# Kernel tuning notes

Measured on AMD Instinct MI355X. Metric: run time of the kernel, lower is better.

The kernel has to match this reference:

```python
import jax, jax.numpy as jnp
import numpy as np

N = 50000      # nodes
E = 800000     # edges
G = 2000       # graphs
F_IN = 34
HID = 256
H = 8
D = 32         # HID // H
L = 5


def _layer_norm(x, g, b, eps=1e-5):
    m = x.mean(-1, keepdims=True)
    v = ((x - m) ** 2).mean(-1, keepdims=True)
    return (x - m) / jnp.sqrt(v + eps) * g + b


def _gelu(x):
    return jax.nn.gelu(x, approximate=False)  # torch exact GELU


def _segment_softmax(scores, seg, n):
    # scores: [E', H], seg: [E'] target node ids
    m = jax.ops.segment_max(scores, seg, num_segments=n)
    m = jnp.where(jnp.isfinite(m), m, 0.0)
    ex = jnp.exp(scores - m[seg])
    den = jax.ops.segment_sum(ex, seg, num_segments=n)
    return ex / (den[seg] + 1e-16)


def setup_inputs() -> dict:
    key = jax.random.key(0)
    ks = iter(jax.random.split(key, 64))

    def p(shape, fan):
        return (jax.random.normal(next(ks), shape, jnp.float32) / np.sqrt(fan)).astype(jnp.float32)

    inp = {}
    inp['x'] = jax.random.normal(next(ks), (N, F_IN), jnp.float32)
    inp['edge_index'] = jax.random.randint(next(ks), (2, E), 0, N, jnp.int32)
    inp['batch'] = jnp.sort(jax.random.randint(next(ks), (N,), 0, G, jnp.int32))

    # input embed
    inp['in_W'] = p((F_IN, HID), F_IN); inp['in_b'] = jnp.zeros((HID,), jnp.float32)
    inp['in_ln_g'] = jnp.ones((HID,), jnp.float32); inp['in_ln_b'] = jnp.zeros((HID,), jnp.float32)
    # 5 GATv2 layers (stacked on leading dim)
    inp['gat_Wl'] = p((L, HID, HID), HID); inp['gat_bl'] = jnp.zeros((L, HID), jnp.float32)
    inp['gat_Wr'] = p((L, HID, HID), HID); inp['gat_br'] = jnp.zeros((L, HID), jnp.float32)
    inp['gat_att'] = p((L, H, D), D)
    inp['gat_bias'] = jnp.zeros((L, HID), jnp.float32)
    inp['gat_ln_g'] = jnp.ones((L, HID), jnp.float32); inp['gat_ln_b'] = jnp.zeros((L, HID), jnp.float32)
    # TransformerConv
    inp['tr_Wq'] = p((HID, HID), HID); inp['tr_bq'] = jnp.zeros((HID,), jnp.float32)
    inp['tr_Wk'] = p((HID, HID), HID); inp['tr_bk'] = jnp.zeros((HID,), jnp.float32)
    inp['tr_Wv'] = p((HID, HID), HID); inp['tr_bv'] = jnp.zeros((HID,), jnp.float32)
    inp['tr_Wskip'] = p((HID, HID), HID); inp['tr_bskip'] = jnp.zeros((HID,), jnp.float32)
    inp['tr_ln_g'] = jnp.ones((HID,), jnp.float32); inp['tr_ln_b'] = jnp.zeros((HID,), jnp.float32)
    # output proj
    inp['out_W'] = p((2 * HID, 2 * HID), 2 * HID); inp['out_b'] = jnp.zeros((2 * HID,), jnp.float32)
    inp['out_ln_g'] = jnp.ones((2 * HID,), jnp.float32); inp['out_ln_b'] = jnp.zeros((2 * HID,), jnp.float32)
    return inp


def reference(x, edge_index, batch,
              in_W, in_b, in_ln_g, in_ln_b,
              gat_Wl, gat_bl, gat_Wr, gat_br, gat_att, gat_bias, gat_ln_g, gat_ln_b,
              tr_Wq, tr_bq, tr_Wk, tr_bk, tr_Wv, tr_bv, tr_Wskip, tr_bskip, tr_ln_g, tr_ln_b,
              out_W, out_b, out_ln_g, out_ln_b):
    # input embedding (dropout inactive in eval)
    h = _gelu(_layer_norm(x @ in_W + in_b, in_ln_g, in_ln_b))

    src, dst = edge_index[0], edge_index[1]  # PyG: row=source j, col=target i
    loops = jnp.arange(N, dtype=src.dtype)
    s2 = jnp.concatenate([src, loops])  # GATv2 adds self loops
    d2 = jnp.concatenate([dst, loops])

    for l in range(L):  # small fixed loop over layers
        xl = (h @ gat_Wl[l] + gat_bl[l]).reshape(N, H, D)  # source transform / message
        xr = (h @ gat_Wr[l] + gat_br[l]).reshape(N, H, D)  # target transform
        e = jax.nn.leaky_relu(xl[s2] + xr[d2], 0.2)        # [E', H, D]
        score = jnp.einsum('ehd,hd->eh', e, gat_att[l])
        alpha = _segment_softmax(score, d2, N)             # softmax over incoming edges
        out = jax.ops.segment_sum(xl[s2] * alpha[..., None], d2, num_segments=N)
        out = out.reshape(N, HID) + gat_bias[l]
        h = h + _gelu(_layer_norm(out, gat_ln_g[l], gat_ln_b[l]))

    # TransformerConv (no self loops, root_weight skip connection)
    q = (h @ tr_Wq + tr_bq).reshape(N, H, D)
    k = (h @ tr_Wk + tr_bk).reshape(N, H, D)
    v = (h @ tr_Wv + tr_bv).reshape(N, H, D)
    score = (q[dst] * k[src]).sum(-1) / jnp.sqrt(jnp.float32(D))  # [E, H]
    alpha = _segment_softmax(score, dst, N)
    out = jax.ops.segment_sum(v[src] * alpha[..., None], dst, num_segments=N).reshape(N, HID)
    out = out + h @ tr_Wskip + tr_bskip
    h = h + _layer_norm(out, tr_ln_g, tr_ln_b)

    # global mean + max pool
    cnt = jax.ops.segment_sum(jnp.ones((N,), h.dtype), batch, num_segments=G)
    h_mean = jax.ops.segment_sum(h, batch, num_segments=G) / jnp.maximum(cnt, 1.0)[:, None]
    h_max = jax.ops.segment_max(h, batch, num_segments=G)
    h_max = jnp.where(jnp.isfinite(h_max), h_max, 0.0)
    ge = jnp.concatenate([h_mean, h_max], axis=-1)  # [G, 512]
    return _gelu(_layer_norm(ge @ out_W + out_b, out_ln_g, out_ln_b))
```

## Files before the change

kernel.cpp:

```cpp
#include <hip/hip_runtime.h>
#include <math.h>

#define N_NODES 50000
#define N_EDGES 800000
#define N_GRAPH 2000
#define F_INPUT 34
#define HID 256
#define NLAYER 5

typedef __attribute__((ext_vector_type(8))) short short8;
typedef __attribute__((ext_vector_type(4))) float float4v;

__device__ __forceinline__ float gelu_f(float x) {
  return 0.5f * x * (1.0f + erff(x * 0.70710678118654752440f));
}
__device__ __forceinline__ unsigned short bfr(float f) {
  unsigned u = __float_as_uint(f);
  return (unsigned short)((u + 0x7fffu + ((u >> 16) & 1u)) >> 16);
}
__device__ __forceinline__ float b2f(unsigned short s) {
  return __uint_as_float(((unsigned)s) << 16);
}
__device__ __forceinline__ float4 ld4bf(const unsigned short* p) {
  ushort4 u = *(const ushort4*)p;
  float4 f;
  f.x = b2f(u.x); f.y = b2f(u.y); f.z = b2f(u.z); f.w = b2f(u.w);
  return f;
}
__device__ __forceinline__ void acp16(const unsigned short* g, unsigned short* l) {
  __builtin_amdgcn_global_load_lds(
      (const __attribute__((address_space(1))) void*)g,
      (__attribute__((address_space(3))) void*)l, 16, 0, 0);
}

__global__ __launch_bounds__(256) void gemm_bias(
    const float* __restrict__ A, const float* __restrict__ B,
    const float* __restrict__ bias, float* __restrict__ C,
    int M, int Nn, int K) {
  __shared__ float As[16][64];
  __shared__ float Bs[16][64];
  int tid = threadIdx.x;
  int tx = tid & 15, ty = tid >> 4;
  int row0 = blockIdx.y * 64;
  int col0 = blockIdx.x * 64;
  float acc[4][4] = {};
  int a_r = tid >> 2;
  int a_c = (tid & 3) * 4;
  int b_r = tid >> 4;
  int b_c = (tid & 15) * 4;

  for (int k0 = 0; k0 < K; k0 += 16) {
    int ar = row0 + a_r;
#pragma unroll
    for (int i = 0; i < 4; ++i) {
      int kc = k0 + a_c + i;
      As[a_c + i][a_r] = (ar < M && kc < K) ? A[(long)ar * K + kc] : 0.f;
    }
    int bk = k0 + b_r;
    if (bk < K) {
      float4 bv = *(const float4*)&B[(long)bk * Nn + col0 + b_c];
      Bs[b_r][b_c + 0] = bv.x; Bs[b_r][b_c + 1] = bv.y;
      Bs[b_r][b_c + 2] = bv.z; Bs[b_r][b_c + 3] = bv.w;
    } else {
      Bs[b_r][b_c + 0] = 0.f; Bs[b_r][b_c + 1] = 0.f;
      Bs[b_r][b_c + 2] = 0.f; Bs[b_r][b_c + 3] = 0.f;
    }
    __syncthreads();
#pragma unroll
    for (int kk = 0; kk < 16; ++kk) {
      float4 a = *(const float4*)&As[kk][ty * 4];
      float4 b = *(const float4*)&Bs[kk][tx * 4];
      float av[4] = {a.x, a.y, a.z, a.w};
      float bv[4] = {b.x, b.y, b.z, b.w};
#pragma unroll
      for (int i = 0; i < 4; ++i)
#pragma unroll
        for (int j = 0; j < 4; ++j) acc[i][j] += av[i] * bv[j];
    }
    __syncthreads();
  }
  float4 bi = *(const float4*)&bias[col0 + tx * 4];
  float bia[4] = {bi.x, bi.y, bi.z, bi.w};
#pragma unroll
  for (int i = 0; i < 4; ++i) {
    int r = row0 + ty * 4 + i;
    if (r < M) {
      float4 o;
      o.x = acc[i][0] + bia[0]; o.y = acc[i][1] + bia[1];
      o.z = acc[i][2] + bia[2]; o.w = acc[i][3] + bia[3];
      *(float4*)&C[(long)r * Nn + col0 + tx * 4] = o;
    }
  }
}

__global__ __launch_bounds__(256) void gemm_mfma(
    const unsigned short* __restrict__ A, const unsigned short* __restrict__ Bt,
    const float* __restrict__ bias, void* __restrict__ Cv,
    int M, int Nn, int K, int flags) {
  __shared__ unsigned short smem[12288];
  unsigned short* As = smem;
  unsigned short* Bs = smem + 4096;
  int tid = threadIdx.x;
  int wave = tid >> 6, lane = tid & 63;
  int row0 = blockIdx.y * 128;
  int col0 = blockIdx.x * 128;
  int wm0 = (wave >> 1) * 64;
  int wn0 = (wave & 1) * 64;
  int q = lane >> 4;
  int ln = lane & 15;

  int srow = wave * 16 + (lane >> 2);
  int scol = (lane & 3) * 8;
  int ra0 = min(row0 + srow, M - 1);
  int ra1 = min(row0 + srow + 64, M - 1);
  const unsigned short* pa0 = A + (size_t)ra0 * K + scol;
  const unsigned short* pa1 = A + (size_t)ra1 * K + scol;
  const unsigned short* pb0 = Bt + (size_t)(col0 + srow) * K + scol;
  const unsigned short* pb1 = Bt + (size_t)(col0 + srow + 64) * K + scol;
  unsigned short* la0 = As + wave * 512;
  unsigned short* la1 = As + wave * 512 + 2048;
  unsigned short* lb0 = Bs + wave * 512;
  unsigned short* lb1 = Bs + wave * 512 + 2048;

  float4v acc[4][4];
#pragma unroll
  for (int i = 0; i < 4; ++i)
#pragma unroll
    for (int j = 0; j < 4; ++j) acc[i][j] = (float4v)0.f;

  for (int k0 = 0; k0 < K; k0 += 32) {
    acp16(pa0 + k0, la0);
    acp16(pa1 + k0, la1);
    acp16(pb0 + k0, lb0);
    acp16(pb1 + k0, lb1);
    __syncthreads();
    short8 af[4], bf[4];
#pragma unroll
    for (int i = 0; i < 4; ++i)
      af[i] = *(const short8*)&As[(wm0 + i * 16 + ln) * 32 + q * 8];
#pragma unroll
    for (int j = 0; j < 4; ++j)
      bf[j] = *(const short8*)&Bs[(wn0 + j * 16 + ln) * 32 + q * 8];
#pragma unroll
    for (int i = 0; i < 4; ++i)
#pragma unroll
      for (int j = 0; j < 4; ++j)
        acc[i][j] = __builtin_amdgcn_mfma_f32_16x16x32_bf16(af[i], bf[j], acc[i][j], 0, 0, 0);
    __syncthreads();
  }
  int rb = (lane >> 4) * 4;
  if (flags & 2) {
    unsigned short* Cb = (unsigned short*)Cv;
    unsigned short* eb = smem + wave * 2560;
#pragma unroll
    for (int p = 0; p < 2; ++p) {
#pragma unroll
      for (int jj = 0; jj < 2; ++jj) {
        int j = p * 2 + jj;
        float bv = bias[col0 + wn0 + j * 16 + ln];
#pragma unroll
        for (int i = 0; i < 4; ++i)
#pragma unroll
          for (int r = 0; r < 4; ++r)
            eb[(i * 16 + rb + r) * 40 + jj * 16 + ln] = bfr(acc[i][j][r] + bv);
      }
      int grow = row0 + wm0 + lane;
      uint4 w0 = *(uint4*)&eb[lane * 40 + 0];
      uint4 w1 = *(uint4*)&eb[lane * 40 + 8];
      uint4 w2 = *(uint4*)&eb[lane * 40 + 16];
      uint4 w3 = *(uint4*)&eb[lane * 40 + 24];
      if (grow < M) {
        unsigned short* dst = Cb + (size_t)grow * Nn + col0 + wn0 + p * 32;
        *(uint4*)&dst[0] = w0;
        *(uint4*)&dst[8] = w1;
        *(uint4*)&dst[16] = w2;
        *(uint4*)&dst[24] = w3;
      }
    }
  } else {
    float* C = (float*)Cv;
#pragma unroll
    for (int j = 0; j < 4; ++j) {
      int col = col0 + wn0 + j * 16 + ln;
      float bv = bias[col];
#pragma unroll
      for (int i = 0; i < 4; ++i)
#pragma unroll
        for (int r = 0; r < 4; ++r) {
          int row = row0 + wm0 + i * 16 + rb + r;
          if (row < M) C[(size_t)row * Nn + col] = acc[i][j][r] + bv;
        }
    }
  }
}

__global__ __launch_bounds__(256) void prep_w(
    const float* __restrict__ Wl, const float* __restrict__ Wr,
    const float* __restrict__ Wq, const float* __restrict__ Wk,
    const float* __restrict__ Wv, const float* __restrict__ Wsk,
    unsigned short* __restrict__ out) {
  __shared__ float t[32][33];
  int m = blockIdx.z;
  const float* W = (m < 10) ? (((m & 1) ? Wr : Wl) + (size_t)(m >> 1) * 65536)
                 : (m == 10) ? Wq : (m == 11) ? Wk : (m == 12) ? Wv : Wsk;
  int k0 = blockIdx.y * 32, n0 = blockIdx.x * 32;
  int r = threadIdx.x >> 5, c = threadIdx.x & 31;
  for (int rr = r; rr < 32; rr += 8)
    t[rr][c] = W[(size_t)(k0 + rr) * HID + n0 + c];
  __syncthreads();
  unsigned short* o = out + (size_t)m * 65536;
  for (int rr = r; rr < 32; rr += 8)
    o[(size_t)(n0 + rr) * HID + k0 + c] = bfr(t[c][rr]);
}

__global__ __launch_bounds__(256) void prep_wout(const float* __restrict__ W,
                                                 unsigned short* __restrict__ o) {
  __shared__ float t[32][33];
  int k0 = blockIdx.y * 32, n0 = blockIdx.x * 32;
  int r = threadIdx.x >> 5, c = threadIdx.x & 31;
  for (int rr = r; rr < 32; rr += 8)
    t[rr][c] = W[(size_t)(k0 + rr) * 512 + n0 + c];
  __syncthreads();
  for (int rr = r; rr < 32; rr += 8)
    o[(size_t)(n0 + rr) * 512 + k0 + c] = bfr(t[c][rr]);
}

__global__ __launch_bounds__(256) void prep_bias(
    const float* __restrict__ bl, const float* __restrict__ br,
    const float* __restrict__ bq, const float* __restrict__ bk,
    const float* __restrict__ bv, float* __restrict__ out) {
  int i = blockIdx.x * 256 + threadIdx.x;
  if (i < 2560) {
    int l = i >> 9, c = i & 511;
    out[i] = (c < 256) ? bl[l * 256 + c] : br[l * 256 + (c - 256)];
  } else if (i < 3328) {
    int j = i - 2560;
    out[i] = (j < 256) ? bq[j] : (j < 512) ? bk[j - 256] : bv[j - 512];
  }
}

__global__ __launch_bounds__(256) void ln_act(
    const float* __restrict__ in, const float* __restrict__ gam,
    const float* __restrict__ bet, float* __restrict__ out,
    unsigned short* __restrict__ outb,
    int n_rows, int width, int do_gelu) {
  int wid = blockIdx.x * 4 + (threadIdx.x >> 6);
  int lane = threadIdx.x & 63;
  if (wid >= n_rows) return;
  int chunks = width >> 8;
  float4 v[2];
  float s = 0.f;
  for (int c = 0; c < chunks; ++c) {
    int off = c * 256 + lane * 4;
    float4 t = *(const float4*)&in[(size_t)wid * width + off];
    v[c] = t;
    s += t.x + t.y + t.z + t.w;
  }
  for (int o = 1; o < 64; o <<= 1) s += __shfl_xor(s, o);
  float mean = s / (float)width;
  float vs = 0.f;
  for (int c = 0; c < chunks; ++c) {
    float dx = v[c].x - mean, dy = v[c].y - mean, dz = v[c].z - mean, dw = v[c].w - mean;
    vs += dx * dx + dy * dy + dz * dz + dw * dw;
  }
  for (int o = 1; o < 64; o <<= 1) vs += __shfl_xor(vs, o);
  float inv = rsqrtf(vs / (float)width + 1e-5f);
  for (int c = 0; c < chunks; ++c) {
    int off = c * 256 + lane * 4;
    float4 g4 = *(const float4*)&gam[off];
    float4 b4 = *(const float4*)&bet[off];
    float y[4] = {(v[c].x - mean) * inv * g4.x + b4.x,
                  (v[c].y - mean) * inv * g4.y + b4.y,
                  (v[c].z - mean) * inv * g4.z + b4.z,
                  (v[c].w - mean) * inv * g4.w + b4.w};
    if (do_gelu) {
#pragma unroll
      for (int i = 0; i < 4; ++i) y[i] = gelu_f(y[i]);
    }
    size_t idx = (size_t)wid * width + off;
    float4 o4 = {y[0], y[1], y[2], y[3]};
    *(float4*)&out[idx] = o4;
    if (outb) {
      ushort4 ob = {bfr(y[0]), bfr(y[1]), bfr(y[2]), bfr(y[3])};
      *(ushort4*)&outb[idx] = ob;
    }
  }
}

__global__ __launch_bounds__(256) void edge_count(const int* __restrict__ ei,
                                                  int* __restrict__ counts) {
  int e = blockIdx.x * 256 + threadIdx.x;
  if (e < N_EDGES) atomicAdd(&counts[ei[N_EDGES + e]], 1);
}

__global__ __launch_bounds__(1024) void scan1(const int* __restrict__ counts,
                                              int* __restrict__ indptr,
                                              int* __restrict__ bsums, int n) {
  __shared__ int sm[1024];
  int tid = threadIdx.x;
  int i = blockIdx.x * 1024 + tid;
  int v = (i < n) ? counts[i] : 0;
  sm[tid] = v;
  __syncthreads();
  for (int off = 1; off < 1024; off <<= 1) {
    int t = (tid >= off) ? sm[tid - off] : 0;
    __syncthreads();
    sm[tid] += t;
    __syncthreads();
  }
  if (i < n) indptr[i] = sm[tid] - v;
  if (tid == 1023) bsums[blockIdx.x] = sm[1023];
}

__global__ void scan2(int* __restrict__ bsums, int nb) {
  if (threadIdx.x == 0 && blockIdx.x == 0) {
    int acc = 0;
    for (int i = 0; i < nb; ++i) { int t = bsums[i]; bsums[i] = acc; acc += t; }
  }
}

__global__ __launch_bounds__(256) void scan3(const int* __restrict__ bsums,
                                             int* __restrict__ indptr,
                                             int* __restrict__ cursor, int n) {
  int i = blockIdx.x * 256 + threadIdx.x;
  if (i < n) {
    int v = indptr[i] + bsums[i >> 10];
    indptr[i] = v;
    cursor[i] = v;
  }
  if (i == 0) indptr[n] = N_EDGES;
}

__global__ __launch_bounds__(256) void edge_scatter(const int* __restrict__ ei,
                                                    int* __restrict__ cursor,
                                                    int* __restrict__ esrc) {
  int e = blockIdx.x * 256 + threadIdx.x;
  if (e < N_EDGES) {
    int d = ei[N_EDGES + e];
    int p = atomicAdd(&cursor[d], 1);
    esrc[p] = ei[e];
  }
}

#define GAT_EDGE(f)                                                        \
  {                                                                        \
    float ex = f.x + xri.x; ex = ex > 0.f ? ex : 0.2f * ex;                \
    float ey = f.y + xri.y; ey = ey > 0.f ? ey : 0.2f * ey;                \
    float ez = f.z + xri.z; ez = ez > 0.f ? ez : 0.2f * ez;                \
    float ew = f.w + xri.w; ew = ew > 0.f ? ew : 0.2f * ew;                \
    float p = ex * a4.x + ey * a4.y + ez * a4.z + ew * a4.w;               \
    p += __shfl_xor(p, 1); p += __shfl_xor(p, 2); p += __shfl_xor(p, 4);   \
    float wgt = __expf(fminf(p - m0, 60.f));                               \
    ax += wgt * f.x; ay += wgt * f.y; az += wgt * f.z; aw += wgt * f.w;    \
    lsum += wgt;                                                           \
  }

__global__ __launch_bounds__(256) void gat_agg(
    const unsigned short* __restrict__ xlr, const float* __restrict__ att,
    const int* __restrict__ indptr, const int* __restrict__ esrc,
    const float* __restrict__ pre_bias, const float* __restrict__ gam,
    const float* __restrict__ bet, float* __restrict__ h,
    unsigned short* __restrict__ hb) {
  int wid = blockIdx.x * 4 + (threadIdx.x >> 6);
  int lane = threadIdx.x & 63;
  if (wid >= N_NODES) return;
  float4 xri = ld4bf(&xlr[(size_t)wid * 512 + 256 + lane * 4]);
  float4 a4 = *(const float4*)&att[lane * 4];
  int beg = indptr[wid], end = indptr[wid + 1];

  float m0, lsum, ax, ay, az, aw;
  {
    float4 f = ld4bf(&xlr[(size_t)wid * 512 + lane * 4]);
    float ex = f.x + xri.x; ex = ex > 0.f ? ex : 0.2f * ex;
    float ey = f.y + xri.y; ey = ey > 0.f ? ey : 0.2f * ey;
    float ez = f.z + xri.z; ez = ez > 0.f ? ez : 0.2f * ez;
    float ew = f.w + xri.w; ew = ew > 0.f ? ew : 0.2f * ew;
    float p = ex * a4.x + ey * a4.y + ez * a4.z + ew * a4.w;
    p += __shfl_xor(p, 1); p += __shfl_xor(p, 2); p += __shfl_xor(p, 4);
    m0 = p; lsum = 1.f;
    ax = f.x; ay = f.y; az = f.z; aw = f.w;
  }
  int e = beg;
  for (; e + 3 < end; e += 4) {
    int j0 = esrc[e], j1 = esrc[e + 1], j2 = esrc[e + 2], j3 = esrc[e + 3];
    float4 f0 = ld4bf(&xlr[(size_t)j0 * 512 + lane * 4]);
    float4 f1 = ld4bf(&xlr[(size_t)j1 * 512 + lane * 4]);
    float4 f2 = ld4bf(&xlr[(size_t)j2 * 512 + lane * 4]);
    float4 f3 = ld4bf(&xlr[(size_t)j3 * 512 + lane * 4]);
    GAT_EDGE(f0); GAT_EDGE(f1); GAT_EDGE(f2); GAT_EDGE(f3);
  }
  for (; e < end; ++e) {
    int j = esrc[e];
    float4 f = ld4bf(&xlr[(size_t)j * 512 + lane * 4]);
    GAT_EDGE(f);
  }
  float inv = 1.f / (lsum + 1e-16f);
  float4 pb = *(const float4*)&pre_bias[lane * 4];
  float y0 = ax * inv + pb.x, y1 = ay * inv + pb.y;
  float y2 = az * inv + pb.z, y3 = aw * inv + pb.w;
  float s = y0 + y1 + y2 + y3;
  for (int o = 1; o < 64; o <<= 1) s += __shfl_xor(s, o);
  float mean = s * (1.f / 256.f);
  float d0 = y0 - mean, d1 = y1 - mean, d2 = y2 - mean, d3 = y3 - mean;
  float vs = d0 * d0 + d1 * d1 + d2 * d2 + d3 * d3;
  for (int o = 1; o < 64; o <<= 1) vs += __shfl_xor(vs, o);
  float inv2 = rsqrtf(vs * (1.f / 256.f) + 1e-5f);
  float4 g4 = *(const float4*)&gam[lane * 4];
  float4 b4 = *(const float4*)&bet[lane * 4];
  y0 = gelu_f(d0 * inv2 * g4.x + b4.x);
  y1 = gelu_f(d1 * inv2 * g4.y + b4.y);
  y2 = gelu_f(d2 * inv2 * g4.z + b4.z);
  y3 = gelu_f(d3 * inv2 * g4.w + b4.w);
  size_t idx = (size_t)wid * HID + lane * 4;
  float4 r4 = *(const float4*)&h[idx];
  y0 += r4.x; y1 += r4.y; y2 += r4.z; y3 += r4.w;
  float4 o4 = {y0, y1, y2, y3};
  *(float4*)&h[idx] = o4;
  ushort4 ob = {bfr(y0), bfr(y1), bfr(y2), bfr(y3)};
  *(ushort4*)&hb[idx] = ob;
}

#define TR_EDGE(kj, vj)                                                    \
  {                                                                        \
    float p = qi.x * kj.x + qi.y * kj.y + qi.z * kj.z + qi.w * kj.w;       \
    p += __shfl_xor(p, 1); p += __shfl_xor(p, 2); p += __shfl_xor(p, 4);   \
    float wgt = __expf(fminf(p * scale, 60.f));                            \
    ax += wgt * vj.x; ay += wgt * vj.y; az += wgt * vj.z; aw += wgt * vj.w;\
    lsum += wgt;                                                           \
  }

__global__ __launch_bounds__(256) void tr_agg(
    const unsigned short* __restrict__ qkv, const int* __restrict__ indptr,
    const int* __restrict__ esrc, const unsigned short* __restrict__ skipb,
    const float* __restrict__ gam, const float* __restrict__ bet,
    float* __restrict__ h) {
  int wid = blockIdx.x * 4 + (threadIdx.x >> 6);
  int lane = threadIdx.x & 63;
  if (wid >= N_NODES) return;
  float4 qi = ld4bf(&qkv[(size_t)wid * 768 + lane * 4]);
  int beg = indptr[wid], end = indptr[wid + 1];
  float lsum = 0.f;
  float ax = 0.f, ay = 0.f, az = 0.f, aw = 0.f;
  const float scale = 0.17677669529663687f;
  int e = beg;
  for (; e + 1 < end; e += 2) {
    int j0 = esrc[e], j1 = esrc[e + 1];
    float4 k0 = ld4bf(&qkv[(size_t)j0 * 768 + 256 + lane * 4]);
    float4 v0 = ld4bf(&qkv[(size_t)j0 * 768 + 512 + lane * 4]);
    float4 k1 = ld4bf(&qkv[(size_t)j1 * 768 + 256 + lane * 4]);
    float4 v1 = ld4bf(&qkv[(size_t)j1 * 768 + 512 + lane * 4]);
    TR_EDGE(k0, v0); TR_EDGE(k1, v1);
  }
  if (e < end) {
    int j = esrc[e];
    float4 kj = ld4bf(&qkv[(size_t)j * 768 + 256 + lane * 4]);
    float4 vj = ld4bf(&qkv[(size_t)j * 768 + 512 + lane * 4]);
    TR_EDGE(kj, vj);
  }
  float inv = 1.f / (lsum + 1e-16f);
  size_t idx = (size_t)wid * HID + lane * 4;
  float4 sk = ld4bf(&skipb[idx]);
  float y0 = ax * inv + sk.x, y1 = ay * inv + sk.y;
  float y2 = az * inv + sk.z, y3 = aw * inv + sk.w;
  float s = y0 + y1 + y2 + y3;
  for (int o = 1; o < 64; o <<= 1) s += __shfl_xor(s, o);
  float mean = s * (1.f / 256.f);
  float d0 = y0 - mean, d1 = y1 - mean, d2 = y2 - mean, d3 = y3 - mean;
  float vs = d0 * d0 + d1 * d1 + d2 * d2 + d3 * d3;
  for (int o = 1; o < 64; o <<= 1) vs += __shfl_xor(vs, o);
  float inv2 = rsqrtf(vs * (1.f / 256.f) + 1e-5f);
  float4 g4 = *(const float4*)&gam[lane * 4];
  float4 b4 = *(const float4*)&bet[lane * 4];
  float4 r4 = *(const float4*)&h[idx];
  float4 o4;
  o4.x = r4.x + d0 * inv2 * g4.x + b4.x;
  o4.y = r4.y + d1 * inv2 * g4.y + b4.y;
  o4.z = r4.z + d2 * inv2 * g4.z + b4.z;
  o4.w = r4.w + d3 * inv2 * g4.w + b4.w;
  *(float4*)&h[idx] = o4;
}

__global__ __launch_bounds__(256) void graph_bounds(const int* __restrict__ batch,
                                                    int* __restrict__ gptr) {
  int i = blockIdx.x * 256 + threadIdx.x;
  if (i >= N_NODES) return;
  int b0 = batch[i];
  if (i == 0)
    for (int g = 0; g <= b0; ++g) gptr[g] = 0;
  int b1 = (i + 1 < N_NODES) ? batch[i + 1] : N_GRAPH;
  for (int g = b0 + 1; g <= b1; ++g) gptr[g] = i + 1;
}

__global__ __launch_bounds__(256) void pool_seg(
    const float* __restrict__ h, const int* __restrict__ gptr,
    unsigned short* __restrict__ geb) {
  int g = blockIdx.x, c = threadIdx.x;
  int s = gptr[g], e = gptr[g + 1];
  float sum = 0.f, mx = -INFINITY;
  for (int r = s; r < e; ++r) {
    float vv = h[(size_t)r * HID + c];
    sum += vv;
    mx = fmaxf(mx, vv);
  }
  int cnt = e - s;
  geb[(size_t)g * 512 + c] = bfr(sum / (float)max(cnt, 1));
  geb[(size_t)g * 512 + 256 + c] = bfr(cnt ? mx : 0.f);
}

static inline void mfma_launch(const unsigned short* A, const unsigned short* Bt,
                               const float* bias, void* C, int M, int Nn, int K,
                               int flags, hipStream_t s) {
  dim3 grid(Nn / 128, (M + 127) / 128);
  gemm_mfma<<<grid, 256, 0, s>>>(A, Bt, bias, C, M, Nn, K, flags);
}

extern "C" void kernel_launch(void* const* d_in, const int* in_sizes, int n_in,
                              void* d_out, int out_size, void* d_ws, size_t ws_size,
                              hipStream_t stream) {
  const float* x       = (const float*)d_in[0];
  const int*   ei      = (const int*)d_in[1];
  const int*   batch   = (const int*)d_in[2];
  const float* in_W    = (const float*)d_in[3];
  const float* in_b    = (const float*)d_in[4];
  const float* in_ln_g = (const float*)d_in[5];
  const float* in_ln_b = (const float*)d_in[6];
  const float* gat_Wl  = (const float*)d_in[7];
  const float* gat_bl  = (const float*)d_in[8];
  const float* gat_Wr  = (const float*)d_in[9];
  const float* gat_br  = (const float*)d_in[10];
  const float* gat_att = (const float*)d_in[11];
  const float* gat_bias= (const float*)d_in[12];
  const float* gat_ln_g= (const float*)d_in[13];
  const float* gat_ln_b= (const float*)d_in[14];
  const float* tr_Wq   = (const float*)d_in[15];
  const float* tr_bq   = (const float*)d_in[16];
  const float* tr_Wk   = (const float*)d_in[17];
  const float* tr_bk   = (const float*)d_in[18];
  const float* tr_Wv   = (const float*)d_in[19];
  const float* tr_bv   = (const float*)d_in[20];
  const float* tr_Wsk  = (const float*)d_in[21];
  const float* tr_bsk  = (const float*)d_in[22];
  const float* tr_ln_g = (const float*)d_in[23];
  const float* tr_ln_b = (const float*)d_in[24];
  const float* out_W   = (const float*)d_in[25];
  const float* out_b   = (const float*)d_in[26];
  const float* out_ln_g= (const float*)d_in[27];
  const float* out_ln_b= (const float*)d_in[28];

  char* w = (char*)d_ws;
  auto take = [&](size_t bytes) -> char* {
    char* p = w;
    w += (bytes + 255) & ~(size_t)255;
    return p;
  };
  const size_t NB = (size_t)N_NODES * HID * sizeof(float);
  float* h    = (float*)take(NB);
  float* aggO = (float*)take(NB);
  unsigned short* hb  = (unsigned short*)take((size_t)N_NODES * HID * 2);
  unsigned short* xq  = (unsigned short*)take((size_t)N_NODES * 768 * 2);
  unsigned short* wbuf= (unsigned short*)take((size_t)(14 * 65536 + 262144) * 2);
  float* bcat = (float*)take(3328 * sizeof(float));
  int* indptr = (int*)take((N_NODES + 1) * sizeof(int));
  int* cursor = (int*)take(N_NODES * sizeof(int));
  int* counts = (int*)take(N_NODES * sizeof(int));
  int* esrc   = (int*)take(N_EDGES * sizeof(int));
  int* bsums  = (int*)take(64 * sizeof(int));
  unsigned short* skipb = (unsigned short*)aggO;
  char* w2 = (char*)xq;
  auto take2 = [&](size_t bytes) -> char* {
    char* p = w2;
    w2 += (bytes + 255) & ~(size_t)255;
    return p;
  };
  int* gptr = (int*)take2((N_GRAPH + 1) * sizeof(int));
  unsigned short* geb = (unsigned short*)take2((size_t)N_GRAPH * 512 * 2);
  float* tbuf = (float*)take2((size_t)N_GRAPH * 512 * sizeof(float));

  const int EB = (N_EDGES + 255) / 256;
  const int WB = (N_NODES + 3) / 4;
  const int NSB = (N_NODES + 1023) / 1024;

  {
    dim3 g(8, 8, 14);
    prep_w<<<g, 256, 0, stream>>>(gat_Wl, gat_Wr, tr_Wq, tr_Wk, tr_Wv, tr_Wsk, wbuf);
    dim3 g2(16, 16);
    prep_wout<<<g2, 256, 0, stream>>>(out_W, wbuf + (size_t)14 * 65536);
    prep_bias<<<13, 256, 0, stream>>>(gat_bl, gat_br, tr_bq, tr_bk, tr_bv, bcat);
  }

  hipMemsetAsync(counts, 0, N_NODES * sizeof(int), stream);
  edge_count<<<EB, 256, 0, stream>>>(ei, counts);
  scan1<<<NSB, 1024, 0, stream>>>(counts, indptr, bsums, N_NODES);
  scan2<<<1, 64, 0, stream>>>(bsums, NSB);
  scan3<<<(N_NODES + 255) / 256, 256, 0, stream>>>(bsums, indptr, cursor, N_NODES);
  edge_scatter<<<EB, 256, 0, stream>>>(ei, cursor, esrc);

  {
    dim3 grid(HID / 64, (N_NODES + 63) / 64);
    gemm_bias<<<grid, 256, 0, stream>>>(x, in_W, in_b, aggO, N_NODES, HID, F_INPUT);
  }
  ln_act<<<WB, 256, 0, stream>>>(aggO, in_ln_g, in_ln_b, h, hb, N_NODES, HID, 1);

  for (int l = 0; l < NLAYER; ++l) {
    mfma_launch(hb, wbuf + (size_t)(2 * l) * 65536, bcat + l * 512, xq,
                N_NODES, 512, HID, 2, stream);
    gat_agg<<<WB, 256, 0, stream>>>(xq, gat_att + l * HID, indptr, esrc,
                                    gat_bias + l * HID, gat_ln_g + l * HID,
                                    gat_ln_b + l * HID, h, hb);
  }

  mfma_launch(hb, wbuf + (size_t)13 * 65536, tr_bsk, skipb,
              N_NODES, HID, HID, 2, stream);
  mfma_launch(hb, wbuf + (size_t)10 * 65536, bcat + 2560, xq,
              N_NODES, 768, HID, 2, stream);
  tr_agg<<<WB, 256, 0, stream>>>(xq, indptr, esrc, skipb, tr_ln_g, tr_ln_b, h);

  graph_bounds<<<(N_NODES + 255) / 256, 256, 0, stream>>>(batch, gptr);
  pool_seg<<<N_GRAPH, 256, 0, stream>>>(h, gptr, geb);

  mfma_launch(geb, wbuf + (size_t)14 * 65536, out_b, tbuf,
              N_GRAPH, 512, 512, 0, stream);
  ln_act<<<(N_GRAPH + 3) / 4, 256, 0, stream>>>(tbuf, out_ln_g, out_ln_b,
                                                (float*)d_out, nullptr,
                                                N_GRAPH, 512, 1);
}
```

Baseline: 1.182 ms.

## Interleave K/V weights for single 16-byte gathers and deepen GAT edge unroll

Reorders the K and V projection weight rows and biases so that each lane's 4 K values and 4 V values for a node sit next to each other. The transformer aggregation can then fetch both with one 16-byte load per edge instead of two 8-byte loads, and its edge loop is unrolled by 4. The query is pre-scaled once, and the GAT aggregation gets an 8-wide unrolled edge loop plus fmax-based leaky ReLU and FMAs. The aim is fewer memory transactions and more loads in flight for the gather-bound edge loops, at the cost of higher register pressure.

```diff
diff --git a/kernel.cpp b/kernel.cpp
--- a/kernel.cpp
+++ b/kernel.cpp
@@ -20,6 +20,12 @@
 }
 __device__ __forceinline__ float b2f(unsigned short s) {
   return __uint_as_float(((unsigned)s) << 16);
+}
+__device__ __forceinline__ float b2f_lo(unsigned u) {
+  return __uint_as_float(u << 16);
+}
+__device__ __forceinline__ float b2f_hi(unsigned u) {
+  return __uint_as_float(u & 0xffff0000u);
 }
 __device__ __forceinline__ float4 ld4bf(const unsigned short* p) {
   ushort4 u = *(const ushort4*)p;
@@ -208,9 +214,14 @@
   for (int rr = r; rr < 32; rr += 8)
     t[rr][c] = W[(size_t)(k0 + rr) * HID + n0 + c];
   __syncthreads();
-  unsigned short* o = out + (size_t)m * 65536;
-  for (int rr = r; rr < 32; rr += 8)
-    o[(size_t)(n0 + rr) * HID + k0 + c] = bfr(t[c][rr]);
+  for (int rr = r; rr < 32; rr += 8) {
+    int n = n0 + rr;
+    size_t row;
+    if (m == 11)      row = 11 * 256 + (size_t)((n >> 2) * 8 + (n & 3));
+    else if (m == 12) row = 11 * 256 + (size_t)((n >> 2) * 8 + 4 + (n & 3));
+    else              row = (size_t)m * 256 + n;
+    out[row * HID + k0 + c] = bfr(t[c][rr]);
+  }
 }
 
 __global__ __launch_bounds__(256) void prep_wout(const float* __restrict__ W,
@@ -235,7 +246,15 @@
     out[i] = (c < 256) ? bl[l * 256 + c] : br[l * 256 + (c - 256)];
   } else if (i < 3328) {
     int j = i - 2560;
-    out[i] = (j < 256) ? bq[j] : (j < 512) ? bk[j - 256] : bv[j - 512];
+    float v;
+    if (j < 256) {
+      v = bq[j];
+    } else {
+      int p = j - 256;
+      int hi = p >> 3, lo = p & 7;
+      v = (lo < 4) ? bk[hi * 4 + lo] : bv[hi * 4 + (lo - 4)];
+    }
+    out[i] = v;
   }
 }
 
@@ -344,14 +363,15 @@
 
 #define GAT_EDGE(f)                                                        \
   {                                                                        \
-    float ex = f.x + xri.x; ex = ex > 0.f ? ex : 0.2f * ex;                \
-    float ey = f.y + xri.y; ey = ey > 0.f ? ey : 0.2f * ey;                \
-    float ez = f.z + xri.z; ez = ez > 0.f ? ez : 0.2f * ez;                \
-    float ew = f.w + xri.w; ew = ew > 0.f ? ew : 0.2f * ew;                \
+    float ex = f.x + xri.x; ex = fmaxf(ex, 0.2f * ex);                     \
+    float ey = f.y + xri.y; ey = fmaxf(ey, 0.2f * ey);                     \
+    float ez = f.z + xri.z; ez = fmaxf(ez, 0.2f * ez);                     \
+    float ew = f.w + xri.w; ew = fmaxf(ew, 0.2f * ew);                     \
     float p = ex * a4.x + ey * a4.y + ez * a4.z + ew * a4.w;               \
     p += __shfl_xor(p, 1); p += __shfl_xor(p, 2); p += __shfl_xor(p, 4);   \
     float wgt = __expf(fminf(p - m0, 60.f));                               \
-    ax += wgt * f.x; ay += wgt * f.y; az += wgt * f.z; aw += wgt * f.w;    \
+    ax = fmaf(wgt, f.x, ax); ay = fmaf(wgt, f.y, ay);                      \
+    az = fmaf(wgt, f.z, az); aw = fmaf(wgt, f.w, aw);                      \
     lsum += wgt;                                                           \
   }
 
@@ -371,27 +391,42 @@
   float m0, lsum, ax, ay, az, aw;
   {
     float4 f = ld4bf(&xlr[(size_t)wid * 512 + lane * 4]);
-    float ex = f.x + xri.x; ex = ex > 0.f ? ex : 0.2f * ex;
-    float ey = f.y + xri.y; ey = ey > 0.f ? ey : 0.2f * ey;
-    float ez = f.z + xri.z; ez = ez > 0.f ? ez : 0.2f * ez;
-    float ew = f.w + xri.w; ew = ew > 0.f ? ew : 0.2f * ew;
+    float ex = f.x + xri.x; ex = fmaxf(ex, 0.2f * ex);
+    float ey = f.y + xri.y; ey = fmaxf(ey, 0.2f * ey);
+    float ez = f.z + xri.z; ez = fmaxf(ez, 0.2f * ez);
+    float ew = f.w + xri.w; ew = fmaxf(ew, 0.2f * ew);
     float p = ex * a4.x + ey * a4.y + ez * a4.z + ew * a4.w;
     p += __shfl_xor(p, 1); p += __shfl_xor(p, 2); p += __shfl_xor(p, 4);
     m0 = p; lsum = 1.f;
     ax = f.x; ay = f.y; az = f.z; aw = f.w;
   }
+  const unsigned short* xbase = xlr + lane * 4;
   int e = beg;
+  for (; e + 7 < end; e += 8) {
+    int j0 = esrc[e],     j1 = esrc[e + 1], j2 = esrc[e + 2], j3 = esrc[e + 3];
+    int j4 = esrc[e + 4], j5 = esrc[e + 5], j6 = esrc[e + 6], j7 = esrc[e + 7];
+    float4 f0 = ld4bf(xbase + (size_t)j0 * 512);
+    float4 f1 = ld4bf(xbase + (size_t)j1 * 512);
+    float4 f2 = ld4bf(xbase + (size_t)j2 * 512);
+    float4 f3 = ld4bf(xbase + (size_t)j3 * 512);
+    float4 f4 = ld4bf(xbase + (size_t)j4 * 512);
+    float4 f5 = ld4bf(xbase + (size_t)j5 * 512);
+    float4 f6 = ld4bf(xbase + (size_t)j6 * 512);
+    float4 f7 = ld4bf(xbase + (size_t)j7 * 512);
+    GAT_EDGE(f0); GAT_EDGE(f1); GAT_EDGE(f2); GAT_EDGE(f3);
+    GAT_EDGE(f4); GAT_EDGE(f5); GAT_EDGE(f6); GAT_EDGE(f7);
+  }
   for (; e + 3 < end; e += 4) {
     int j0 = esrc[e], j1 = esrc[e + 1], j2 = esrc[e + 2], j3 = esrc[e + 3];
-    float4 f0 = ld4bf(&xlr[(size_t)j0 * 512 + lane * 4]);
-    float4 f1 = ld4bf(&xlr[(size_t)j1 * 512 + lane * 4]);
-    float4 f2 = ld4bf(&xlr[(size_t)j2 * 512 + lane * 4]);
-    float4 f3 = ld4bf(&xlr[(size_t)j3 * 512 + lane * 4]);
+    float4 f0 = ld4bf(xbase + (size_t)j0 * 512);
+    float4 f1 = ld4bf(xbase + (size_t)j1 * 512);
+    float4 f2 = ld4bf(xbase + (size_t)j2 * 512);
+    float4 f3 = ld4bf(xbase + (size_t)j3 * 512);
     GAT_EDGE(f0); GAT_EDGE(f1); GAT_EDGE(f2); GAT_EDGE(f3);
   }
   for (; e < end; ++e) {
     int j = esrc[e];
-    float4 f = ld4bf(&xlr[(size_t)j * 512 + lane * 4]);
+    float4 f = ld4bf(xbase + (size_t)j * 512);
     GAT_EDGE(f);
   }
   float inv = 1.f / (lsum + 1e-16f);
@@ -420,13 +455,17 @@
   *(ushort4*)&hb[idx] = ob;
 }
 
-#define TR_EDGE(kj, vj)                                                    \
-  {                                                                        \
-    float p = qi.x * kj.x + qi.y * kj.y + qi.z * kj.z + qi.w * kj.w;       \
-    p += __shfl_xor(p, 1); p += __shfl_xor(p, 2); p += __shfl_xor(p, 4);   \
-    float wgt = __expf(fminf(p * scale, 60.f));                            \
-    ax += wgt * vj.x; ay += wgt * vj.y; az += wgt * vj.z; aw += wgt * vj.w;\
-    lsum += wgt;                                                           \
+#define TR_EDGE(u_)                                                         \
+  {                                                                         \
+    float p = qi.x * b2f_lo(u_.x);                                          \
+    p = fmaf(qi.y, b2f_hi(u_.x), p);                                        \
+    p = fmaf(qi.z, b2f_lo(u_.y), p);                                        \
+    p = fmaf(qi.w, b2f_hi(u_.y), p);                                        \
+    p += __shfl_xor(p, 1); p += __shfl_xor(p, 2); p += __shfl_xor(p, 4);    \
+    float wgt = __expf(fminf(p, 60.f));                                     \
+    ax = fmaf(wgt, b2f_lo(u_.z), ax); ay = fmaf(wgt, b2f_hi(u_.z), ay);     \
+    az = fmaf(wgt, b2f_lo(u_.w), az); aw = fmaf(wgt, b2f_hi(u_.w), aw);     \
+    lsum += wgt;                                                            \
   }
 
 __global__ __launch_bounds__(256) void tr_agg(
@@ -437,25 +476,25 @@
   int wid = blockIdx.x * 4 + (threadIdx.x >> 6);
   int lane = threadIdx.x & 63;
   if (wid >= N_NODES) return;
+  const float scale = 0.17677669529663687f;
   float4 qi = ld4bf(&qkv[(size_t)wid * 768 + lane * 4]);
+  qi.x *= scale; qi.y *= scale; qi.z *= scale; qi.w *= scale;
+  const unsigned short* kvbase = qkv + 256 + lane * 8;
   int beg = indptr[wid], end = indptr[wid + 1];
   float lsum = 0.f;
   float ax = 0.f, ay = 0.f, az = 0.f, aw = 0.f;
-  const float scale = 0.17677669529663687f;
   int e = beg;
-  for (; e + 1 < end; e += 2) {
-    int j0 = esrc[e], j1 = esrc[e + 1];
-    float4 k0 = ld4bf(&qkv[(size_t)j0 * 768 + 256 + lane * 4]);
-    float4 v0 = ld4bf(&qkv[(size_t)j0 * 768 + 512 + lane * 4]);
-    float4 k1 = ld4bf(&qkv[(size_t)j1 * 768 + 256 + lane * 4]);
-    float4 v1 = ld4bf(&qkv[(size_t)j1 * 768 + 512 + lane * 4]);
-    TR_EDGE(k0, v0); TR_EDGE(k1, v1);
-  }
-  if (e < end) {
-    int j = esrc[e];
-    float4 kj = ld4bf(&qkv[(size_t)j * 768 + 256 + lane * 4]);
-    float4 vj = ld4bf(&qkv[(size_t)j * 768 + 512 + lane * 4]);
-    TR_EDGE(kj, vj);
+  for (; e + 3 < end; e += 4) {
+    int j0 = esrc[e], j1 = esrc[e + 1], j2 = esrc[e + 2], j3 = esrc[e + 3];
+    uint4 u0 = *(const uint4*)(kvbase + (size_t)j0 * 768);
+    uint4 u1 = *(const uint4*)(kvbase + (size_t)j1 * 768);
+    uint4 u2 = *(const uint4*)(kvbase + (size_t)j2 * 768);
+    uint4 u3 = *(const uint4*)(kvbase + (size_t)j3 * 768);
+    TR_EDGE(u0); TR_EDGE(u1); TR_EDGE(u2); TR_EDGE(u3);
+  }
+  for (; e < end; ++e) {
+    uint4 u0 = *(const uint4*)(kvbase + (size_t)esrc[e] * 768);
+    TR_EDGE(u0);
   }
   float inv = 1.f / (lsum + 1e-16f);
   size_t idx = (size_t)wid * HID + lane * 4;
```

Measured after the change: 1.290 ms. +9.1%, slower.
